# Performance work log

Measured on AMD Instinct MI355X. Metric: run time of the kernel, lower is better.

Reference implementation:

```python
import jax, jax.numpy as jnp
import numpy as np

# ----- problem dimensions (must match setup_inputs) -----
B = 50          # graphs per batch
NPG = 2000      # nodes per graph (equal-size graphs)
N = B * NPG     # total nodes = 100_000
D = 128         # in_channels
E = 600_000     # total edges
EA = 16         # edge_attr_dim
RATIO = 0.5
K = int(RATIO * NPG)  # nodes kept per graph = 1000
EPS = 1e-6


def setup_inputs() -> dict:
    key = jax.random.key(0)
    ks = jax.random.split(key, 12)
    x = jax.random.normal(ks[0], (N, D), jnp.float32)
    # edges constrained within graphs (each graph owns a contiguous node block)
    eg = jax.random.randint(ks[1], (E,), 0, B)
    src = eg * NPG + jax.random.randint(ks[2], (E,), 0, NPG)
    dst = eg * NPG + jax.random.randint(ks[3], (E,), 0, NPG)
    edge_index = jnp.stack([src, dst]).astype(jnp.int32)
    edge_attr = jax.random.normal(ks[4], (E, EA), jnp.float32)
    batch = (jnp.arange(N) // NPG).astype(jnp.int32)
    # feat_mlp: Linear(D,D) -> ReLU -> Linear(D,1)
    W1 = jax.random.normal(ks[5], (D, D), jnp.float32) / np.sqrt(D)
    b1 = jnp.zeros((D,), jnp.float32)
    W2 = jax.random.normal(ks[6], (D, 1), jnp.float32) / np.sqrt(D)
    b2 = jnp.zeros((1,), jnp.float32)
    # edge_mlp: Linear(EA,D) -> ReLU -> Linear(D,1)
    We1 = jax.random.normal(ks[7], (EA, D), jnp.float32) / np.sqrt(EA)
    be1 = jnp.zeros((D,), jnp.float32)
    We2 = jax.random.normal(ks[8], (D, 1), jnp.float32) / np.sqrt(D)
    be2 = jnp.zeros((1,), jnp.float32)
    view_weight = jnp.ones((3,), jnp.float32)
    return {"x": x, "edge_index": edge_index, "edge_attr": edge_attr,
            "batch": batch, "W1": W1, "b1": b1, "W2": W2, "b2": b2,
            "We1": We1, "be1": be1, "We2": We2, "be2": be2,
            "view_weight": view_weight}


def _standardize(v):
    # torch .std() is unbiased (ddof=1)
    return (v - v.mean()) / (jnp.std(v, ddof=1) + EPS)


def _scores(x, src, dst, edge_attr, W1, b1, W2, b2, We1, be1, We2, be2, vw):
    # edge weights: softplus(edge_mlp(edge_attr)) + eps
    ew = jax.nn.softplus((jax.nn.relu(edge_attr @ We1 + be1) @ We2 + be2)[:, 0]) + EPS
    deg_w = jnp.zeros((N,), x.dtype).at[src].add(ew)
    dis = jnp.where(deg_w > 0, deg_w ** -0.5, 0.0)
    norm = dis[src] * ew * dis[dst]                       # [E]
    x_diff = jnp.zeros_like(x).at[src].add(x[dst] * norm[:, None])  # [N,D]
    # view 1: structural (log degree)
    deg_c = jnp.zeros((N,), x.dtype).at[src].add(1.0)
    struct_score = _standardize(jnp.log(deg_c + 1.0))
    # view 2: feature MLP
    feat_raw = (jax.nn.relu(x @ W1 + b1) @ W2 + b2)[:, 0]
    feat_score = _standardize(feat_raw)
    # view 3: diffusion cosine similarity
    dot = jnp.sum(x * x_diff, axis=-1)
    cos = dot / ((jnp.linalg.norm(x, axis=-1) + EPS) *
                 (jnp.linalg.norm(x_diff, axis=-1) + EPS))
    diff_score = _standardize(cos)
    raw = jnp.stack([struct_score, feat_score, diff_score], axis=-1) @ vw
    return jax.nn.sigmoid(raw)                            # [N]


def reference(x, edge_index, edge_attr, batch, W1, b1, W2, b2,
              We1, be1, We2, be2, view_weight):
    src, dst = edge_index[0], edge_index[1]
    score = _scores(x, src, dst, edge_attr, W1, b1, W2, b2,
                    We1, be1, We2, be2, view_weight)
    # vectorized per-graph top-k (graphs are equal-size contiguous blocks)
    loc = jax.lax.top_k(score.reshape(B, NPG), K)[1]      # [B,K] local indices
    keep = (jnp.arange(B, dtype=loc.dtype)[:, None] * NPG + loc).reshape(-1)  # [B*K]
    node_mask = jnp.zeros((N,), bool).at[keep].set(True)
    new_id = jnp.full((N,), -1, jnp.int32).at[keep].set(
        jnp.arange(B * K, dtype=jnp.int32))
    e_mask = node_mask[src] & node_mask[dst]              # [E]
    out_edge_index = jnp.where(e_mask[None, :],
                               jnp.stack([new_id[src], new_id[dst]]), 0)
    out_edge_attr = jnp.where(e_mask[:, None], edge_attr, 0.0)
    out_x = x[keep] * score[keep][:, None]                # [B*K, D]
    out_batch = (jnp.arange(B * K) // K).astype(batch.dtype)
    return out_x, out_edge_index, out_edge_attr, out_batch, e_mask
```

## Files before the change

kernel.cpp:

```cpp
#include <hip/hip_runtime.h>
#include <math.h>

#define NN   100000
#define DD   128
#define EE   600000
#define EAD  16
#define BB   50
#define NPG  2000
#define KK   1000
#define NKEEP (BB*KK)

#define OFF_OEI    6400000
#define OFF_OEA    7600000
#define OFF_OBATCH 17200000
#define OFF_EMASK  17250000

#define NRED 240
#define SCAN_NB 98

#define EPB 1024
__global__ __launch_bounds__(256) void k_edge_mlp(
    const float* __restrict__ edge_attr, const int* __restrict__ src,
    const float* __restrict__ We1, const float* __restrict__ be1,
    const float* __restrict__ We2, const float* __restrict__ be2,
    float* __restrict__ ew, float* __restrict__ deg_w, float* __restrict__ deg_c)
{
    __shared__ float wt[2048];
    __shared__ float b1s[128];
    __shared__ float w2s[128];
    for (int idx = threadIdx.x; idx < 2048; idx += 256) {
        int j = idx >> 4, k = idx & 15;
        wt[idx] = We1[k * DD + j];
    }
    if (threadIdx.x < 128) {
        b1s[threadIdx.x] = be1[threadIdx.x];
        w2s[threadIdx.x] = We2[threadIdx.x];
    }
    __syncthreads();

    int e0 = blockIdx.x * EPB + threadIdx.x;
    float ea[4][16];
    #pragma unroll
    for (int i = 0; i < 4; i++) {
        int e = e0 + 256 * i; if (e >= EE) e = EE - 1;
        const float4* ap = (const float4*)(edge_attr + (size_t)e * EAD);
        float4 a0 = ap[0], a1 = ap[1], a2 = ap[2], a3 = ap[3];
        ea[i][0]=a0.x; ea[i][1]=a0.y; ea[i][2]=a0.z; ea[i][3]=a0.w;
        ea[i][4]=a1.x; ea[i][5]=a1.y; ea[i][6]=a1.z; ea[i][7]=a1.w;
        ea[i][8]=a2.x; ea[i][9]=a2.y; ea[i][10]=a2.z; ea[i][11]=a2.w;
        ea[i][12]=a3.x; ea[i][13]=a3.y; ea[i][14]=a3.z; ea[i][15]=a3.w;
    }
    float acc[4] = {0.f, 0.f, 0.f, 0.f};
    for (int j = 0; j < DD; j++) {
        float4 w0 = *(const float4*)(wt + j*16);
        float4 w1 = *(const float4*)(wt + j*16 + 4);
        float4 w2 = *(const float4*)(wt + j*16 + 8);
        float4 w3 = *(const float4*)(wt + j*16 + 12);
        float bj = b1s[j], w2j = w2s[j];
        #pragma unroll
        for (int i = 0; i < 4; i++) {
            float h = bj;
            h += ea[i][0]*w0.x;  h += ea[i][1]*w0.y;
            h += ea[i][2]*w0.z;  h += ea[i][3]*w0.w;
            h += ea[i][4]*w1.x;  h += ea[i][5]*w1.y;
            h += ea[i][6]*w1.z;  h += ea[i][7]*w1.w;
            h += ea[i][8]*w2.x;  h += ea[i][9]*w2.y;
            h += ea[i][10]*w2.z; h += ea[i][11]*w2.w;
            h += ea[i][12]*w3.x; h += ea[i][13]*w3.y;
            h += ea[i][14]*w3.z; h += ea[i][15]*w3.w;
            acc[i] += fmaxf(h, 0.f) * w2j;
        }
    }
    float bias2 = be2[0];
    #pragma unroll
    for (int i = 0; i < 4; i++) {
        int e = e0 + 256 * i;
        if (e < EE) {
            float a = acc[i] + bias2;
            float sp = fmaxf(a, 0.f) + log1pf(expf(-fabsf(a)));
            float w = sp + 1e-6f;
            ew[e] = w;
            int s = src[e];
            atomicAdd(&deg_w[s], w);
            atomicAdd(&deg_c[s], 1.0f);
        }
    }
}

__global__ __launch_bounds__(256) void k_dis(const float* __restrict__ deg_w,
                                             float* __restrict__ dis)
{
    int n = blockIdx.x * 256 + threadIdx.x;
    if (n >= NN) return;
    float d = deg_w[n];
    dis[n] = d > 0.f ? 1.f / sqrtf(d) : 0.f;
}

__global__ __launch_bounds__(1024) void k_scan_block(
    const float* __restrict__ deg_c, int* __restrict__ scanned,
    int* __restrict__ blocksums)
{
    __shared__ int s[1024];
    int i = blockIdx.x * 1024 + threadIdx.x;
    int c = (i < NN) ? (int)deg_c[i] : 0;
    s[threadIdx.x] = c;
    __syncthreads();
    for (int off = 1; off < 1024; off <<= 1) {
        int v = (threadIdx.x >= off) ? s[threadIdx.x - off] : 0;
        __syncthreads();
        s[threadIdx.x] += v;
        __syncthreads();
    }
    if (i < NN) scanned[i] = s[threadIdx.x] - c;
    if (threadIdx.x == 1023) blocksums[blockIdx.x] = s[1023];
}

__global__ __launch_bounds__(128) void k_scan_top(int* __restrict__ blocksums)
{
    __shared__ int s[128];
    int c = (threadIdx.x < SCAN_NB) ? blocksums[threadIdx.x] : 0;
    s[threadIdx.x] = c;
    __syncthreads();
    for (int off = 1; off < 128; off <<= 1) {
        int v = (threadIdx.x >= off) ? s[threadIdx.x - off] : 0;
        __syncthreads();
        s[threadIdx.x] += v;
        __syncthreads();
    }
    if (threadIdx.x < SCAN_NB) blocksums[threadIdx.x] = s[threadIdx.x] - c;
}

__global__ __launch_bounds__(256) void k_cursor(
    const int* __restrict__ scanned, const int* __restrict__ blocksums,
    int* __restrict__ rowstart, int* __restrict__ cur)
{
    int n = blockIdx.x * 256 + threadIdx.x;
    if (n >= NN) return;
    int st = scanned[n] + blocksums[n >> 10];
    rowstart[n] = st;
    cur[n] = st;
}

__global__ __launch_bounds__(256) void k_scatter(
    const int* __restrict__ src, const int* __restrict__ dst,
    const float* __restrict__ ew, const float* __restrict__ dis,
    int* __restrict__ cur, int* __restrict__ csr_dst, float* __restrict__ csr_w)
{
    int e = blockIdx.x * 256 + threadIdx.x;
    if (e >= EE) return;
    int s = src[e], d = dst[e];
    float w = dis[s] * ew[e] * dis[d];
    int pos = atomicAdd(&cur[s], 1);
    csr_dst[pos] = d;
    csr_w[pos] = w;
}

__global__ __launch_bounds__(256) void k_gather_cos(
    const int* __restrict__ rowstart, const float* __restrict__ deg_c,
    const int* __restrict__ csr_dst, const float* __restrict__ csr_w,
    const float* __restrict__ x, float* __restrict__ raw0, float* __restrict__ raw2)
{
    int node = (blockIdx.x * 256 + threadIdx.x) >> 6;
    int lane = threadIdx.x & 63;
    if (node >= NN) return;
    int start = rowstart[node];
    int deg = (int)deg_c[node];
    const float2* xp = (const float2*)x;
    float2 xn = xp[(size_t)node * 64 + lane];
    float2 acc = {0.f, 0.f};
    for (int base = 0; base < deg; base += 64) {
        int rem = deg - base; if (rem > 64) rem = 64;
        int md = 0; float mw = 0.f;
        if (lane < rem) {
            md = csr_dst[start + base + lane];
            mw = csr_w[start + base + lane];
        }
        int e = 0;
        for (; e + 4 <= rem; e += 4) {
            int d0 = __shfl(md, e, 64),   d1 = __shfl(md, e+1, 64);
            int d2 = __shfl(md, e+2, 64), d3 = __shfl(md, e+3, 64);
            float w0 = __shfl(mw, e, 64),   w1 = __shfl(mw, e+1, 64);
            float w2 = __shfl(mw, e+2, 64), w3 = __shfl(mw, e+3, 64);
            float2 v0 = xp[(size_t)d0 * 64 + lane];
            float2 v1 = xp[(size_t)d1 * 64 + lane];
            float2 v2 = xp[(size_t)d2 * 64 + lane];
            float2 v3 = xp[(size_t)d3 * 64 + lane];
            acc.x += w0 * v0.x; acc.y += w0 * v0.y;
            acc.x += w1 * v1.x; acc.y += w1 * v1.y;
            acc.x += w2 * v2.x; acc.y += w2 * v2.y;
            acc.x += w3 * v3.x; acc.y += w3 * v3.y;
        }
        for (; e < rem; e++) {
            int d = __shfl(md, e, 64);
            float w = __shfl(mw, e, 64);
            float2 v = xp[(size_t)d * 64 + lane];
            acc.x += w * v.x; acc.y += w * v.y;
        }
    }
    float dot = xn.x * acc.x + xn.y * acc.y;
    float nx  = xn.x * xn.x + xn.y * xn.y;
    float nd  = acc.x * acc.x + acc.y * acc.y;
    #pragma unroll
    for (int off = 32; off; off >>= 1) {
        dot += __shfl_xor(dot, off, 64);
        nx  += __shfl_xor(nx,  off, 64);
        nd  += __shfl_xor(nd,  off, 64);
    }
    if (lane == 0) {
        raw2[node] = dot / ((sqrtf(nx) + 1e-6f) * (sqrtf(nd) + 1e-6f));
        raw0[node] = logf((float)deg + 1.0f);
    }
}

#define XSTR 132
__global__ __launch_bounds__(256) void k_node(
    const float* __restrict__ x,
    const float* __restrict__ W1, const float* __restrict__ b1,
    const float* __restrict__ W2, const float* __restrict__ b2,
    float* __restrict__ raw1)
{
    __shared__ float xs[64 * XSTR];
    int wave = threadIdx.x >> 6, lane = threadIdx.x & 63;
    int ng = lane >> 4, jg = lane & 15;
    int blockBase = blockIdx.x * 64;

    #pragma unroll
    for (int it = 0; it < 8; it++) {
        int s = threadIdx.x + 256 * it;
        int row = s >> 5, c4 = s & 31;
        int gn = blockBase + row; if (gn >= NN) gn = NN - 1;
        *(float4*)(xs + row * XSTR + c4 * 4) =
            *(const float4*)(x + (size_t)gn * DD + c4 * 4);
    }
    __syncthreads();

    const float* xw = xs + (wave * 16 + ng * 4) * XSTR;
    int j0 = jg * 8;
    float acc[4][8];
    #pragma unroll
    for (int i = 0; i < 4; i++)
        #pragma unroll
        for (int jj = 0; jj < 8; jj++) acc[i][jj] = 0.f;

    for (int k = 0; k < DD; k += 4) {
        float4 xv[4];
        #pragma unroll
        for (int i = 0; i < 4; i++) xv[i] = *(const float4*)(xw + i * XSTR + k);
        float4 wv[4][2];
        #pragma unroll
        for (int kk = 0; kk < 4; kk++) {
            wv[kk][0] = *(const float4*)(W1 + (k + kk) * DD + j0);
            wv[kk][1] = *(const float4*)(W1 + (k + kk) * DD + j0 + 4);
        }
        #pragma unroll
        for (int i = 0; i < 4; i++) {
            const float xe[4] = {xv[i].x, xv[i].y, xv[i].z, xv[i].w};
            #pragma unroll
            for (int kk = 0; kk < 4; kk++) {
                acc[i][0] += xe[kk] * wv[kk][0].x;
                acc[i][1] += xe[kk] * wv[kk][0].y;
                acc[i][2] += xe[kk] * wv[kk][0].z;
                acc[i][3] += xe[kk] * wv[kk][0].w;
                acc[i][4] += xe[kk] * wv[kk][1].x;
                acc[i][5] += xe[kk] * wv[kk][1].y;
                acc[i][6] += xe[kk] * wv[kk][1].z;
                acc[i][7] += xe[kk] * wv[kk][1].w;
            }
        }
    }

    float4 b1a = *(const float4*)(b1 + j0), b1b = *(const float4*)(b1 + j0 + 4);
    float4 w2a = *(const float4*)(W2 + j0), w2b = *(const float4*)(W2 + j0 + 4);
    const float b1v[8] = {b1a.x,b1a.y,b1a.z,b1a.w, b1b.x,b1b.y,b1b.z,b1b.w};
    const float w2v[8] = {w2a.x,w2a.y,w2a.z,w2a.w, w2b.x,w2b.y,w2b.z,w2b.w};
    float bias2 = b2[0];
    #pragma unroll
    for (int i = 0; i < 4; i++) {
        float p = 0.f;
        #pragma unroll
        for (int jj = 0; jj < 8; jj++)
            p += fmaxf(acc[i][jj] + b1v[jj], 0.f) * w2v[jj];
        p += __shfl_xor(p, 1, 64);
        p += __shfl_xor(p, 2, 64);
        p += __shfl_xor(p, 4, 64);
        p += __shfl_xor(p, 8, 64);
        int node = blockBase + wave * 16 + ng * 4 + i;
        if (jg == 0 && node < NN) raw1[node] = p + bias2;
    }
}

__global__ __launch_bounds__(256) void k_reduce(
    const float* __restrict__ r0, const float* __restrict__ r1,
    const float* __restrict__ r2, double* __restrict__ partials)
{
    __shared__ double sd[256];
    double s[6] = {0,0,0,0,0,0};
    for (int n = blockIdx.x * 256 + threadIdx.x; n < NN; n += 256 * NRED) {
        double v0 = r0[n], v1 = r1[n], v2 = r2[n];
        s[0] += v0; s[1] += v0*v0;
        s[2] += v1; s[3] += v1*v1;
        s[4] += v2; s[5] += v2*v2;
    }
    for (int q = 0; q < 6; q++) {
        sd[threadIdx.x] = s[q];
        __syncthreads();
        for (int off = 128; off; off >>= 1) {
            if (threadIdx.x < off) sd[threadIdx.x] += sd[threadIdx.x + off];
            __syncthreads();
        }
        if (threadIdx.x == 0) partials[blockIdx.x * 6 + q] = sd[0];
        __syncthreads();
    }
}

__global__ __launch_bounds__(256) void k_stats(const double* __restrict__ partials,
                                               float* __restrict__ stats)
{
    __shared__ double sd[256];
    __shared__ double sums[6];
    for (int q = 0; q < 6; q++) {
        sd[threadIdx.x] = (threadIdx.x < NRED) ? partials[threadIdx.x * 6 + q] : 0.0;
        __syncthreads();
        for (int off = 128; off; off >>= 1) {
            if (threadIdx.x < off) sd[threadIdx.x] += sd[threadIdx.x + off];
            __syncthreads();
        }
        if (threadIdx.x == 0) sums[q] = sd[0];
        __syncthreads();
    }
    if (threadIdx.x == 0) {
        for (int i = 0; i < 3; i++) {
            double sum = sums[2*i], sq = sums[2*i+1];
            double mean = sum / NN;
            double var = (sq - sum * sum / NN) / (NN - 1);
            double sdv = sqrt(var > 0 ? var : 0);
            stats[2*i]   = (float)mean;
            stats[2*i+1] = (float)(1.0 / (sdv + 1e-6));
        }
    }
}

__global__ __launch_bounds__(256) void k_score(
    const float* __restrict__ r0, const float* __restrict__ r1,
    const float* __restrict__ r2, const float* __restrict__ stats,
    const float* __restrict__ vw, float* __restrict__ score)
{
    int n = blockIdx.x * 256 + threadIdx.x;
    if (n >= NN) return;
    float z0 = (r0[n] - stats[0]) * stats[1];
    float z1 = (r1[n] - stats[2]) * stats[3];
    float z2 = (r2[n] - stats[4]) * stats[5];
    float r = z0 * vw[0] + z1 * vw[1] + z2 * vw[2];
    score[n] = 1.f / (1.f + expf(-r));
}

__global__ __launch_bounds__(1024) void k_topk(
    const float* __restrict__ score, int* __restrict__ keep,
    int* __restrict__ new_id, float* __restrict__ obatch)
{
    __shared__ unsigned long long keys[2048];
    int b = blockIdx.x;
    unsigned t = threadIdx.x;
    for (unsigned i = t; i < 2048; i += 1024) {
        unsigned long long kk = 0ull;
        if (i < NPG) {
            float sc = score[b * NPG + i];
            kk = ((unsigned long long)__float_as_uint(sc) << 32)
               | (unsigned long long)(0xFFFFFFFFu - i);
        }
        keys[i] = kk;
    }
    __syncthreads();
    for (unsigned k = 2; k <= 2048; k <<= 1) {
        for (unsigned j = k >> 1; j > 0; j >>= 1) {
            unsigned i = ((t & ~(j - 1)) << 1) | (t & (j - 1));
            unsigned p = i | j;
            unsigned long long a = keys[i], c = keys[p];
            bool up = ((i & k) == 0);
            if ((a < c) == up) { keys[i] = c; keys[p] = a; }
            __syncthreads();
        }
    }
    if (t < KK) {
        unsigned long long kk = keys[t];
        unsigned li = 0xFFFFFFFFu - (unsigned)(kk & 0xFFFFFFFFu);
        int node = b * NPG + (int)li;
        int j = b * KK + (int)t;
        keep[j] = node;
        new_id[node] = j;
        obatch[j] = (float)b;
    }
}

__global__ __launch_bounds__(128) void k_outx(
    const float* __restrict__ x, const float* __restrict__ score,
    const int* __restrict__ keep, float* __restrict__ out_x)
{
    int j = blockIdx.x;
    int node = keep[j];
    float s = score[node];
    out_x[(size_t)j * DD + threadIdx.x] = x[(size_t)node * DD + threadIdx.x] * s;
}

__global__ __launch_bounds__(256) void k_edges(
    const int* __restrict__ src, const int* __restrict__ dst,
    const int* __restrict__ new_id, float* __restrict__ oei,
    float* __restrict__ emask)
{
    int e = blockIdx.x * 256 + threadIdx.x;
    if (e >= EE) return;
    int ns = new_id[src[e]], nd = new_id[dst[e]];
    bool m = (ns >= 0) && (nd >= 0);
    oei[e]      = m ? (float)ns : 0.f;
    oei[EE + e] = m ? (float)nd : 0.f;
    emask[e]    = m ? 1.f : 0.f;
}

__global__ __launch_bounds__(256) void k_attr(
    const float* __restrict__ edge_attr, const float* __restrict__ emask,
    float* __restrict__ oea)
{
    int idx = blockIdx.x * 256 + threadIdx.x;
    if (idx >= EE * 4) return;
    int e = idx >> 2;
    float m = emask[e];
    float4 v = ((const float4*)edge_attr)[idx];
    float4 o; o.x = v.x*m; o.y = v.y*m; o.z = v.z*m; o.w = v.w*m;
    ((float4*)oea)[idx] = o;
}

extern "C" void kernel_launch(void* const* d_in, const int* in_sizes, int n_in,
                              void* d_out, int out_size, void* d_ws, size_t ws_size,
                              hipStream_t stream) {
    const float* x         = (const float*)d_in[0];
    const int*   edge_idx  = (const int*)d_in[1];
    const float* edge_attr = (const float*)d_in[2];
    const float* W1  = (const float*)d_in[4];
    const float* b1  = (const float*)d_in[5];
    const float* W2  = (const float*)d_in[6];
    const float* b2  = (const float*)d_in[7];
    const float* We1 = (const float*)d_in[8];
    const float* be1 = (const float*)d_in[9];
    const float* We2 = (const float*)d_in[10];
    const float* be2 = (const float*)d_in[11];
    const float* vw  = (const float*)d_in[12];

    const int* src = edge_idx;
    const int* dst = edge_idx + EE;

    float* out    = (float*)d_out;
    float* out_x  = out;
    float* oei    = out + OFF_OEI;
    float* oea    = out + OFF_OEA;
    float* obatch = out + OFF_OBATCH;
    float* emask  = out + OFF_EMASK;

    int*   csr_dst   = (int*)(out + 12800000);
    float* csr_w     = out + 13400000;
    int*   rowstart  = (int*)(out + 14000000);
    int*   cur       = (int*)(out + 14100000);
    int*   scanned   = (int*)(out + 14200000);
    int*   blocksums = (int*)(out + 14300000);

    float* ws     = (float*)d_ws;
    float* ew     = ws;
    float* deg_w  = ws + 600000;
    float* deg_c  = ws + 700000;
    float* dis    = ws + 800000;
    float* score  = ws + 900000;
    float* raw0   = ws + 1000000;
    float* raw1   = ws + 1100000;
    float* raw2   = ws + 1200000;
    int*   keep   = (int*)(ws + 1300000);
    int*   new_id = (int*)(ws + 1350000);
    double* partials = (double*)(ws + 1450000);
    float* stats  = ws + 1450000 + 2 * 6 * NRED;

    hipMemsetAsync(deg_w, 0, 2 * NN * sizeof(float), stream);
    hipMemsetAsync(new_id, 0xFF, NN * sizeof(int), stream);

    k_edge_mlp<<<(EE + EPB - 1) / EPB, 256, 0, stream>>>(edge_attr, src, We1, be1,
                                                         We2, be2, ew, deg_w, deg_c);
    k_dis<<<(NN + 255) / 256, 256, 0, stream>>>(deg_w, dis);
    k_scan_block<<<SCAN_NB, 1024, 0, stream>>>(deg_c, scanned, blocksums);
    k_scan_top<<<1, 128, 0, stream>>>(blocksums);
    k_cursor<<<(NN + 255) / 256, 256, 0, stream>>>(scanned, blocksums, rowstart, cur);
    k_scatter<<<(EE + 255) / 256, 256, 0, stream>>>(src, dst, ew, dis, cur, csr_dst, csr_w);
    k_gather_cos<<<(NN * 64 + 255) / 256, 256, 0, stream>>>(rowstart, deg_c, csr_dst,
                                                            csr_w, x, raw0, raw2);
    k_node<<<(NN + 63) / 64, 256, 0, stream>>>(x, W1, b1, W2, b2, raw1);
    k_reduce<<<NRED, 256, 0, stream>>>(raw0, raw1, raw2, partials);
    k_stats<<<1, 256, 0, stream>>>(partials, stats);
    k_score<<<(NN + 255) / 256, 256, 0, stream>>>(raw0, raw1, raw2, stats, vw, score);
    k_topk<<<BB, 1024, 0, stream>>>(score, keep, new_id, obatch);
    k_outx<<<NKEEP, 128, 0, stream>>>(x, score, keep, out_x);
    k_edges<<<(EE + 255) / 256, 256, 0, stream>>>(src, dst, new_id, oei, emask);
    k_attr<<<(EE * 4 + 255) / 256, 256, 0, stream>>>(edge_attr, emask, oea);
}
```

Measured before the change: 452.6 us.

## Restructure edge MLP: register-resident weight slices, shuffle-reduced hidden units, persistent grid

```diff
diff --git a/kernel.cpp b/kernel.cpp
--- a/kernel.cpp
+++ b/kernel.cpp
@@ -18,72 +18,81 @@
 #define NRED 240
 #define SCAN_NB 98
 
-#define EPB 1024
+#define ETILES ((EE + 255) / 256)
+#define EMLP_GRID 1024
 __global__ __launch_bounds__(256) void k_edge_mlp(
     const float* __restrict__ edge_attr, const int* __restrict__ src,
     const float* __restrict__ We1, const float* __restrict__ be1,
     const float* __restrict__ We2, const float* __restrict__ be2,
     float* __restrict__ ew, float* __restrict__ deg_w, float* __restrict__ deg_c)
 {
-    __shared__ float wt[2048];
-    __shared__ float b1s[128];
-    __shared__ float w2s[128];
-    for (int idx = threadIdx.x; idx < 2048; idx += 256) {
-        int j = idx >> 4, k = idx & 15;
-        wt[idx] = We1[k * DD + j];
-    }
-    if (threadIdx.x < 128) {
-        b1s[threadIdx.x] = be1[threadIdx.x];
-        w2s[threadIdx.x] = We2[threadIdx.x];
-    }
-    __syncthreads();
-
-    int e0 = blockIdx.x * EPB + threadIdx.x;
-    float ea[4][16];
+    __shared__ float ea[256 * 16];
+    __shared__ float ptile[256];
+    int lane = threadIdx.x & 63, wv = threadIdx.x >> 6;
+    int jg = lane & 31, es = lane >> 5;
+    int j0 = jg * 4;
+
+    float wr[64];
     #pragma unroll
-    for (int i = 0; i < 4; i++) {
-        int e = e0 + 256 * i; if (e >= EE) e = EE - 1;
-        const float4* ap = (const float4*)(edge_attr + (size_t)e * EAD);
-        float4 a0 = ap[0], a1 = ap[1], a2 = ap[2], a3 = ap[3];
-        ea[i][0]=a0.x; ea[i][1]=a0.y; ea[i][2]=a0.z; ea[i][3]=a0.w;
-        ea[i][4]=a1.x; ea[i][5]=a1.y; ea[i][6]=a1.z; ea[i][7]=a1.w;
-        ea[i][8]=a2.x; ea[i][9]=a2.y; ea[i][10]=a2.z; ea[i][11]=a2.w;
-        ea[i][12]=a3.x; ea[i][13]=a3.y; ea[i][14]=a3.z; ea[i][15]=a3.w;
-    }
-    float acc[4] = {0.f, 0.f, 0.f, 0.f};
-    for (int j = 0; j < DD; j++) {
-        float4 w0 = *(const float4*)(wt + j*16);
-        float4 w1 = *(const float4*)(wt + j*16 + 4);
-        float4 w2 = *(const float4*)(wt + j*16 + 8);
-        float4 w3 = *(const float4*)(wt + j*16 + 12);
-        float bj = b1s[j], w2j = w2s[j];
-        #pragma unroll
-        for (int i = 0; i < 4; i++) {
-            float h = bj;
-            h += ea[i][0]*w0.x;  h += ea[i][1]*w0.y;
-            h += ea[i][2]*w0.z;  h += ea[i][3]*w0.w;
-            h += ea[i][4]*w1.x;  h += ea[i][5]*w1.y;
-            h += ea[i][6]*w1.z;  h += ea[i][7]*w1.w;
-            h += ea[i][8]*w2.x;  h += ea[i][9]*w2.y;
-            h += ea[i][10]*w2.z; h += ea[i][11]*w2.w;
-            h += ea[i][12]*w3.x; h += ea[i][13]*w3.y;
-            h += ea[i][14]*w3.z; h += ea[i][15]*w3.w;
-            acc[i] += fmaxf(h, 0.f) * w2j;
-        }
-    }
+    for (int j = 0; j < 4; j++)
+        #pragma unroll
+        for (int k = 0; k < 16; k++)
+            wr[j * 16 + k] = We1[k * DD + j0 + j];
+    float b1r[4], w2r[4];
+    #pragma unroll
+    for (int j = 0; j < 4; j++) { b1r[j] = be1[j0 + j]; w2r[j] = We2[j0 + j]; }
     float bias2 = be2[0];
-    #pragma unroll
-    for (int i = 0; i < 4; i++) {
-        int e = e0 + 256 * i;
+
+    for (int tile = blockIdx.x; tile < ETILES; tile += EMLP_GRID) {
+        int ebase = tile * 256;
+        #pragma unroll
+        for (int it = 0; it < 4; it++) {
+            int idx = threadIdx.x + 256 * it;
+            long long gidx = (long long)ebase * 4 + idx;
+            long long maxg = (long long)EE * 4;
+            if (gidx >= maxg) gidx = maxg - 1;
+            ((float4*)ea)[idx] = ((const float4*)edge_attr)[gidx];
+        }
+        __syncthreads();
+
+        #pragma unroll 2
+        for (int it = 0; it < 32; it++) {
+            int le = wv * 64 + it * 2 + es;
+            const float* a = ea + le * 16;
+            float4 a0 = *(const float4*)(a);
+            float4 a1 = *(const float4*)(a + 4);
+            float4 a2 = *(const float4*)(a + 8);
+            float4 a3 = *(const float4*)(a + 12);
+            const float av[16] = {a0.x,a0.y,a0.z,a0.w, a1.x,a1.y,a1.z,a1.w,
+                                  a2.x,a2.y,a2.z,a2.w, a3.x,a3.y,a3.z,a3.w};
+            float p = 0.f;
+            #pragma unroll
+            for (int j = 0; j < 4; j++) {
+                float h = b1r[j];
+                #pragma unroll
+                for (int k = 0; k < 16; k++) h += av[k] * wr[j * 16 + k];
+                p += fmaxf(h, 0.f) * w2r[j];
+            }
+            p += __shfl_xor(p, 1, 64);
+            p += __shfl_xor(p, 2, 64);
+            p += __shfl_xor(p, 4, 64);
+            p += __shfl_xor(p, 8, 64);
+            p += __shfl_xor(p, 16, 64);
+            if (jg == 0) ptile[le] = p;
+        }
+        __syncthreads();
+
+        int e = ebase + threadIdx.x;
         if (e < EE) {
-            float a = acc[i] + bias2;
-            float sp = fmaxf(a, 0.f) + log1pf(expf(-fabsf(a)));
+            float acc = ptile[threadIdx.x] + bias2;
+            float sp = fmaxf(acc, 0.f) + log1pf(expf(-fabsf(acc)));
             float w = sp + 1e-6f;
             ew[e] = w;
             int s = src[e];
             atomicAdd(&deg_w[s], w);
             atomicAdd(&deg_c[s], 1.0f);
         }
+        __syncthreads();
     }
 }
 
@@ -479,8 +488,8 @@
     hipMemsetAsync(deg_w, 0, 2 * NN * sizeof(float), stream);
     hipMemsetAsync(new_id, 0xFF, NN * sizeof(int), stream);
 
-    k_edge_mlp<<<(EE + EPB - 1) / EPB, 256, 0, stream>>>(edge_attr, src, We1, be1,
-                                                         We2, be2, ew, deg_w, deg_c);
+    k_edge_mlp<<<EMLP_GRID, 256, 0, stream>>>(edge_attr, src, We1, be1,
+                                              We2, be2, ew, deg_w, deg_c);
     k_dis<<<(NN + 255) / 256, 256, 0, stream>>>(deg_w, dis);
     k_scan_block<<<SCAN_NB, 1024, 0, stream>>>(deg_c, scanned, blocksums);
     k_scan_top<<<1, 128, 0, stream>>>(blocksums);
```

Measured after the change: 435.8 us. -3.7%, faster.

## Stage edge attrs through LDS with coalesced loads; remap gather block order

Applied to the files above, without the earlier changes.

```diff
diff --git a/kernel.cpp b/kernel.cpp
--- a/kernel.cpp
+++ b/kernel.cpp
@@ -18,72 +18,80 @@
 #define NRED 240
 #define SCAN_NB 98
 
-#define EPB 1024
+#define EASTR 20
 __global__ __launch_bounds__(256) void k_edge_mlp(
     const float* __restrict__ edge_attr, const int* __restrict__ src,
     const float* __restrict__ We1, const float* __restrict__ be1,
     const float* __restrict__ We2, const float* __restrict__ be2,
     float* __restrict__ ew, float* __restrict__ deg_w, float* __restrict__ deg_c)
 {
+    __shared__ float ea[256 * EASTR];
     __shared__ float wt[2048];
     __shared__ float b1s[128];
     __shared__ float w2s[128];
-    for (int idx = threadIdx.x; idx < 2048; idx += 256) {
-        int j = idx >> 4, k = idx & 15;
-        wt[idx] = We1[k * DD + j];
-    }
-    if (threadIdx.x < 128) {
-        b1s[threadIdx.x] = be1[threadIdx.x];
-        w2s[threadIdx.x] = We2[threadIdx.x];
+    int tid = threadIdx.x;
+    int ebase = blockIdx.x * 256;
+
+    if (tid < 128) {
+        float tmp[16];
+        #pragma unroll
+        for (int k = 0; k < 16; k++) tmp[k] = We1[k * DD + tid];
+        #pragma unroll
+        for (int c = 0; c < 4; c++)
+            *(float4*)(wt + tid * 16 + c * 4) =
+                make_float4(tmp[4*c], tmp[4*c+1], tmp[4*c+2], tmp[4*c+3]);
+        b1s[tid] = be1[tid];
+        w2s[tid] = We2[tid];
+    }
+    #pragma unroll
+    for (int it = 0; it < 4; it++) {
+        int idx = tid + 256 * it;
+        long long g = (long long)ebase * 4 + idx;
+        long long maxg = (long long)EE * 4;
+        if (g >= maxg) g = maxg - 1;
+        float4 v = ((const float4*)edge_attr)[g];
+        int le = idx >> 2, c = idx & 3;
+        *(float4*)(ea + le * EASTR + c * 4) = v;
     }
     __syncthreads();
 
-    int e0 = blockIdx.x * EPB + threadIdx.x;
-    float ea[4][16];
-    #pragma unroll
-    for (int i = 0; i < 4; i++) {
-        int e = e0 + 256 * i; if (e >= EE) e = EE - 1;
-        const float4* ap = (const float4*)(edge_attr + (size_t)e * EAD);
-        float4 a0 = ap[0], a1 = ap[1], a2 = ap[2], a3 = ap[3];
-        ea[i][0]=a0.x; ea[i][1]=a0.y; ea[i][2]=a0.z; ea[i][3]=a0.w;
-        ea[i][4]=a1.x; ea[i][5]=a1.y; ea[i][6]=a1.z; ea[i][7]=a1.w;
-        ea[i][8]=a2.x; ea[i][9]=a2.y; ea[i][10]=a2.z; ea[i][11]=a2.w;
-        ea[i][12]=a3.x; ea[i][13]=a3.y; ea[i][14]=a3.z; ea[i][15]=a3.w;
-    }
-    float acc[4] = {0.f, 0.f, 0.f, 0.f};
+    float av[16];
+    {
+        const float* a = ea + tid * EASTR;
+        float4 a0 = *(const float4*)(a);
+        float4 a1 = *(const float4*)(a + 4);
+        float4 a2 = *(const float4*)(a + 8);
+        float4 a3 = *(const float4*)(a + 12);
+        av[0]=a0.x; av[1]=a0.y; av[2]=a0.z; av[3]=a0.w;
+        av[4]=a1.x; av[5]=a1.y; av[6]=a1.z; av[7]=a1.w;
+        av[8]=a2.x; av[9]=a2.y; av[10]=a2.z; av[11]=a2.w;
+        av[12]=a3.x; av[13]=a3.y; av[14]=a3.z; av[15]=a3.w;
+    }
+
+    float acc = 0.f;
+    #pragma unroll 4
     for (int j = 0; j < DD; j++) {
-        float4 w0 = *(const float4*)(wt + j*16);
-        float4 w1 = *(const float4*)(wt + j*16 + 4);
-        float4 w2 = *(const float4*)(wt + j*16 + 8);
-        float4 w3 = *(const float4*)(wt + j*16 + 12);
-        float bj = b1s[j], w2j = w2s[j];
-        #pragma unroll
-        for (int i = 0; i < 4; i++) {
-            float h = bj;
-            h += ea[i][0]*w0.x;  h += ea[i][1]*w0.y;
-            h += ea[i][2]*w0.z;  h += ea[i][3]*w0.w;
-            h += ea[i][4]*w1.x;  h += ea[i][5]*w1.y;
-            h += ea[i][6]*w1.z;  h += ea[i][7]*w1.w;
-            h += ea[i][8]*w2.x;  h += ea[i][9]*w2.y;
-            h += ea[i][10]*w2.z; h += ea[i][11]*w2.w;
-            h += ea[i][12]*w3.x; h += ea[i][13]*w3.y;
-            h += ea[i][14]*w3.z; h += ea[i][15]*w3.w;
-            acc[i] += fmaxf(h, 0.f) * w2j;
-        }
-    }
-    float bias2 = be2[0];
-    #pragma unroll
-    for (int i = 0; i < 4; i++) {
-        int e = e0 + 256 * i;
-        if (e < EE) {
-            float a = acc[i] + bias2;
-            float sp = fmaxf(a, 0.f) + log1pf(expf(-fabsf(a)));
-            float w = sp + 1e-6f;
-            ew[e] = w;
-            int s = src[e];
-            atomicAdd(&deg_w[s], w);
-            atomicAdd(&deg_c[s], 1.0f);
-        }
+        float4 w0 = *(const float4*)(wt + j * 16);
+        float4 w1 = *(const float4*)(wt + j * 16 + 4);
+        float4 w2 = *(const float4*)(wt + j * 16 + 8);
+        float4 w3 = *(const float4*)(wt + j * 16 + 12);
+        float h = b1s[j];
+        h += av[0]*w0.x;  h += av[1]*w0.y;  h += av[2]*w0.z;  h += av[3]*w0.w;
+        h += av[4]*w1.x;  h += av[5]*w1.y;  h += av[6]*w1.z;  h += av[7]*w1.w;
+        h += av[8]*w2.x;  h += av[9]*w2.y;  h += av[10]*w2.z; h += av[11]*w2.w;
+        h += av[12]*w3.x; h += av[13]*w3.y; h += av[14]*w3.z; h += av[15]*w3.w;
+        acc += fmaxf(h, 0.f) * w2s[j];
+    }
+
+    int e = ebase + tid;
+    if (e < EE) {
+        float a = acc + be2[0];
+        float sp = fmaxf(a, 0.f) + log1pf(expf(-fabsf(a)));
+        float w = sp + 1e-6f;
+        ew[e] = w;
+        int s = src[e];
+        atomicAdd(&deg_w[s], w);
+        atomicAdd(&deg_c[s], 1.0f);
     }
 }
 
@@ -160,7 +168,8 @@
     const int* __restrict__ csr_dst, const float* __restrict__ csr_w,
     const float* __restrict__ x, float* __restrict__ raw0, float* __restrict__ raw2)
 {
-    int node = (blockIdx.x * 256 + threadIdx.x) >> 6;
+    int blk = blockIdx.x;
+    int node = ((blk & 7) * 3125 + (blk >> 3)) * 4 + (threadIdx.x >> 6);
     int lane = threadIdx.x & 63;
     if (node >= NN) return;
     int start = rowstart[node];
@@ -479,8 +488,8 @@
     hipMemsetAsync(deg_w, 0, 2 * NN * sizeof(float), stream);
     hipMemsetAsync(new_id, 0xFF, NN * sizeof(int), stream);
 
-    k_edge_mlp<<<(EE + EPB - 1) / EPB, 256, 0, stream>>>(edge_attr, src, We1, be1,
-                                                         We2, be2, ew, deg_w, deg_c);
+    k_edge_mlp<<<(EE + 255) / 256, 256, 0, stream>>>(edge_attr, src, We1, be1,
+                                                     We2, be2, ew, deg_w, deg_c);
     k_dis<<<(NN + 255) / 256, 256, 0, stream>>>(deg_w, dis);
     k_scan_block<<<SCAN_NB, 1024, 0, stream>>>(deg_c, scanned, blocksums);
     k_scan_top<<<1, 128, 0, stream>>>(blocksums);
```

Result: faster. 431.6 us (-4.6%).
